# Optimization experiments

Hardware: AMD Instinct MI355X
Metric: run time of the kernel (lower is better)

Reference implementation:

```python
import jax, jax.numpy as jnp
import numpy as np


def setup_inputs() -> dict:
    key = jax.random.key(0)
    n_samples, n_points, dims = 16, 2048, 64
    h = jax.random.normal(key, (n_samples, n_points, dims), dtype=jnp.float32)
    return {"h": h, "K": 16}


def reference(h, K):
    """Pairwise squared distance + K nearest neighbors -> edge list.

    h : (n_samples, n_points, dims)
    Returns (knn_dist, dst, src):
      knn_dist : (n_samples, n_points, K) squared distances to the K nearest points
      dst, src : (n_samples*n_points*K,) int32 globally-offset edge endpoints
    """
    n_samples, n_points, _ = h.shape
    # d[b, i, j] = ||h[b,i]||^2 + ||h[b,j]||^2 - 2 <h[b,i], h[b,j]>
    x2s = jnp.sum(h * h, axis=-1, keepdims=True)          # (s, n, 1)
    d = x2s + jnp.swapaxes(x2s, -1, -2) - 2.0 * jnp.einsum('bnd,bmd->bnm', h, h)
    # smallest-K == top-K of negated distances (matches torch.topk largest=False order)
    neg_vals, k_indices = jax.lax.top_k(-d, K)            # (s, n, K)
    knn_dist = -neg_vals
    # edge list with per-sample node-id offsets (matches the torch flattening)
    src = jnp.broadcast_to(jnp.arange(n_points, dtype=k_indices.dtype)[None, :, None],
                           k_indices.shape)
    offset = (jnp.arange(n_samples, dtype=k_indices.dtype) * n_points)[:, None, None]
    dst = (k_indices + offset).reshape(-1)
    src = (src + offset).reshape(-1)
    return knn_dist, dst, src
```

## Files before the change

kernel.cpp:

```cpp
#include <hip/hip_runtime.h>
#include <hip/hip_fp16.h>
#include <cfloat>


typedef _Float16 half8 __attribute__((ext_vector_type(8)));
typedef float    f32x4 __attribute__((ext_vector_type(4)));

constexpr int NS = 16, NP = 2048, ND = 64, KK = 16;
constexpr int NWV = 4;
constexpr int NT  = NWV * 64;
constexpr int RB  = 32;
constexpr int ITN = RB / 16;
constexpr int JW  = NP / NWV;
constexpr int NJT = JW / 16;
constexpr int MS  = 17;
constexpr int SCB = 36;
constexpr int RCAP = 128;
constexpr int RSTR = RCAP + 1;
constexpr float MARGIN = 1.0f;

__global__ void prep_kernel(const float* __restrict__ h, float* __restrict__ x2,
                            _Float16* __restrict__ hh)
{
    int g = blockIdx.x * 128 + threadIdx.x;
    const float4* row = (const float4*)(h + (size_t)g * ND);
    int ph = g & 15;
    float a0 = 0.f, a1 = 0.f, a2 = 0.f, a3 = 0.f;
    #pragma unroll
    for (int k = 0; k < 16; ++k) {
        float4 v = row[(k + ph) & 15];
        a0 = fmaf(v.x, v.x, a0); a1 = fmaf(v.y, v.y, a1);
        a2 = fmaf(v.z, v.z, a2); a3 = fmaf(v.w, v.w, a3);
    }
    x2[g] = (a0 + a1) + (a2 + a3);
    _Float16* dst = hh + (size_t)g * ND;
    #pragma unroll
    for (int k = 0; k < 8; ++k) {
        float4 v0 = row[2 * k], v1 = row[2 * k + 1];
        half8 p;
        p[0] = (_Float16)v0.x; p[1] = (_Float16)v0.y;
        p[2] = (_Float16)v0.z; p[3] = (_Float16)v0.w;
        p[4] = (_Float16)v1.x; p[5] = (_Float16)v1.y;
        p[6] = (_Float16)v1.z; p[7] = (_Float16)v1.w;
        *(half8*)(dst + k * 8) = p;
    }
}

__device__ __forceinline__ bool lexlt(float a, int ja, float b, int jb)
{
    return (a < b) || (a == b && ja < jb);
}
__device__ __forceinline__ void insert16x(float (&d)[KK], int (&ix)[KK],
                                          float v, int j)
{
    #pragma unroll
    for (int p = KK - 1; p > 0; --p) {
        bool sh = lexlt(v, j, d[p - 1], ix[p - 1]);
        bool he = lexlt(v, j, d[p], ix[p]);
        float nd = sh ? d[p - 1] : (he ? v : d[p]);
        int   ni = sh ? ix[p - 1] : (he ? j : ix[p]);
        d[p] = nd; ix[p] = ni;
    }
    if (lexlt(v, j, d[0], ix[0])) { d[0] = v; ix[0] = j; }
}

__global__ __launch_bounds__(NT, 4)
void knn_mfma(const float* __restrict__ h, const _Float16* __restrict__ hh,
              const float* __restrict__ x2g, float* __restrict__ out)
{
    __shared__ __align__(16) float smem[8672];
    float* ldsx2  = smem;
    float* scb    = smem + 2048;
    float* mw     = smem + 4352;
    float* ldsthr = smem + 4480;
    int*   ring   = (int*)(smem + 4512);
    int*   rcnt   = (int*)(smem + 8640);
    float* md     = scb;
    int*   mi     = (int*)(scb + 1088);

    const int t   = threadIdx.x;
    const int ln  = t & 63;
    const int qd  = ln >> 4;
    const int cl  = ln & 15;
    const int q   = t >> 6;
    const int row = ln & 31;
    const int jh  = ln >> 5;
    const int s   = blockIdx.x >> 6;
    const int rb  = blockIdx.x & 63;
    const int rowbase = rb * RB;
    const float*    __restrict__ hs  = h  + (size_t)s * NP * ND;
    const _Float16* __restrict__ hhs = hh + (size_t)s * NP * ND;

    ((float4*)ldsx2)[t]       = ((const float4*)(x2g + s * NP))[t];
    ((float4*)ldsx2)[t + 256] = ((const float4*)(x2g + s * NP))[t + 256];
    if (t < RB) rcnt[t] = 0;

    half8 afr[ITN][2];
    #pragma unroll
    for (int it = 0; it < ITN; ++it) {
        const _Float16* ap = hhs + (size_t)(rowbase + it * 16 + cl) * ND + qd * 8;
        afr[it][0] = *(const half8*)(ap);
        afr[it][1] = *(const half8*)(ap + 32);
    }
    __syncthreads();

    const int jbase = q * JW;
    float* scbW = scb + q * (16 * SCB);

    float s1 = FLT_MAX, s2 = FLT_MAX, s3 = FLT_MAX, s4 = FLT_MAX;
    const int jro = jh * 8;
    for (int jt = 0; jt < NJT; ++jt) {
        const int j0 = jbase + jt * 16;
        const _Float16* bp = hhs + (size_t)(j0 + cl) * ND + qd * 8;
        half8 blo = *(const half8*)(bp);
        half8 bhi = *(const half8*)(bp + 32);
        float x2j = ldsx2[j0 + cl];

        f32x4 acc[ITN];
        #pragma unroll
        for (int it = 0; it < ITN; ++it) {
            acc[it] = __builtin_amdgcn_mfma_f32_16x16x32_f16(
                          afr[it][0], blo, (f32x4){0.f, 0.f, 0.f, 0.f}, 0, 0, 0);
            acc[it] = __builtin_amdgcn_mfma_f32_16x16x32_f16(
                          afr[it][1], bhi, acc[it], 0, 0, 0);
        }
        #pragma unroll
        for (int it = 0; it < ITN; ++it) {
            f32x4 w;
            #pragma unroll
            for (int r = 0; r < 4; ++r)
                w[r] = fmaf(-2.f, acc[it][r], x2j);
            *(f32x4*)(scbW + cl * SCB + it * 16 + qd * 4) = w;
        }
        #pragma unroll
        for (int u = 0; u < 8; ++u) {
            float v  = scbW[(jro + u) * SCB + row];
            float n1 = fminf(s1, v);
            float n2 = __builtin_amdgcn_fmed3f(s1, s2, v);
            float n3 = __builtin_amdgcn_fmed3f(s2, s3, v);
            float n4 = __builtin_amdgcn_fmed3f(s3, s4, v);
            s1 = n1; s2 = n2; s3 = n3; s4 = n4;
        }
    }
    {
        float o1 = __shfl(s1, row + 32);
        float o2 = __shfl(s2, row + 32);
        float o3 = __shfl(s3, row + 32);
        float o4 = __shfl(s4, row + 32);
        if (ln < 32) {
            float m1 = fminf(s1, o4), m2 = fminf(s2, o3);
            float m3 = fminf(s3, o2), m4 = fminf(s4, o1);
            mw[q * 32 + row] = fmaxf(fmaxf(m1, m2), fmaxf(m3, m4));
        }
    }
    __syncthreads();
    if (q == 0 && ln < 32) {
        float m0 = mw[row], m1 = mw[32 + row];
        float m2 = mw[64 + row], m3 = mw[96 + row];
        ldsthr[row] = fmaxf(fmaxf(m0, m1), fmaxf(m2, m3)) + MARGIN;
    }
    __syncthreads();

    float thrv[ITN * 4];
    #pragma unroll
    for (int it = 0; it < ITN; ++it)
        #pragma unroll
        for (int r = 0; r < 4; ++r)
            thrv[it * 4 + r] = ldsthr[it * 16 + qd * 4 + r];

    for (int jt = 0; jt < NJT; ++jt) {
        const int j0 = jbase + jt * 16;
        const _Float16* bp = hhs + (size_t)(j0 + cl) * ND + qd * 8;
        half8 blo = *(const half8*)(bp);
        half8 bhi = *(const half8*)(bp + 32);
        float x2j = ldsx2[j0 + cl];

        f32x4 acc[ITN];
        #pragma unroll
        for (int it = 0; it < ITN; ++it) {
            acc[it] = __builtin_amdgcn_mfma_f32_16x16x32_f16(
                          afr[it][0], blo, (f32x4){0.f, 0.f, 0.f, 0.f}, 0, 0, 0);
            acc[it] = __builtin_amdgcn_mfma_f32_16x16x32_f16(
                          afr[it][1], bhi, acc[it], 0, 0, 0);
        }
        #pragma unroll
        for (int it = 0; it < ITN; ++it) {
            #pragma unroll
            for (int r = 0; r < 4; ++r) {
                float d2 = fmaf(-2.f, acc[it][r], x2j);
                if (d2 < thrv[it * 4 + r]) {
                    int rw = it * 16 + qd * 4 + r;
                    int slot = atomicAdd(&rcnt[rw], 1);
                    if (slot < RCAP) ring[rw * RSTR + slot] = j0 + cl;
                }
            }
        }
    }
    __syncthreads();

    const int myrow = rowbase + row;
    float4 A[16];
    {
        const float4* ra = (const float4*)(hs + (size_t)myrow * ND);
        #pragma unroll
        for (int k = 0; k < 16; ++k) A[k] = ra[k];
    }
    float x2i;
    {
        float a0 = 0.f, a1 = 0.f, a2 = 0.f, a3 = 0.f;
        #pragma unroll
        for (int k = 0; k < 16; ++k) {
            a0 = fmaf(A[k].x, A[k].x, a0); a1 = fmaf(A[k].y, A[k].y, a1);
            a2 = fmaf(A[k].z, A[k].z, a2); a3 = fmaf(A[k].w, A[k].w, a3);
        }
        x2i = (a0 + a1) + (a2 + a3);
    }
    float dist[KK]; int idx[KK];
    #pragma unroll
    for (int k = 0; k < KK; ++k) { dist[k] = FLT_MAX; idx[k] = 0; }

    const int cntR = min(rcnt[row], RCAP);
    const int w8 = q * 2 + jh;
    #pragma unroll 1
    for (int k = w8; k < cntR; k += 8) {
        int j = ring[row * RSTR + k];
        const float4* cv = (const float4*)(hs + (size_t)j * ND);
        float a0 = 0.f, a1 = 0.f, a2 = 0.f, a3 = 0.f;
        #pragma unroll
        for (int kk = 0; kk < 16; ++kk) {
            float4 c = cv[kk];
            a0 = fmaf(A[kk].x, c.x, a0); a1 = fmaf(A[kk].y, c.y, a1);
            a2 = fmaf(A[kk].z, c.z, a2); a3 = fmaf(A[kk].w, c.w, a3);
        }
        float dotv = (a0 + a1) + (a2 + a3);
        float d2 = fmaf(-2.0f, dotv, x2i + ldsx2[j]);
        if (lexlt(d2, j, dist[KK - 1], idx[KK - 1]))
            insert16x(dist, idx, d2, j);
    }

    #pragma unroll 1
    for (int k = 0; k < KK; ++k) {
        float v  = __shfl(dist[k], row + 32);
        int   jv = __shfl(idx[k],  row + 32);
        bool need = (ln < 32) && lexlt(v, jv, dist[KK - 1], idx[KK - 1]);
        if (!__any(need)) break;
        if (need) insert16x(dist, idx, v, jv);
    }
    __syncthreads();
    #pragma unroll 1
    for (int lvl = 0; lvl < 2; ++lvl) {
        const int step = 1 << lvl;
        const int m    = (step << 1) - 1;
        const bool pub = ((q & m) == step) && ln < 32;
        const int reg  = q >> (lvl + 1);
        if (pub) {
            #pragma unroll
            for (int k = 0; k < KK; ++k) {
                md[(reg * RB + row) * MS + k] = dist[k];
                mi[(reg * RB + row) * MS + k] = idx[k];
            }
        }
        __syncthreads();
        if ((q & m) == 0) {
            #pragma unroll 1
            for (int k = 0; k < KK; ++k) {
                float v  = md[(reg * RB + row) * MS + k];
                int   jv = mi[(reg * RB + row) * MS + k];
                bool need = (ln < 32) && lexlt(v, jv, dist[KK - 1], idx[KK - 1]);
                if (!__any(need)) break;
                if (need) insert16x(dist, idx, v, jv);
            }
        }
        __syncthreads();
    }

    if (q == 0 && ln < 32) {
        const int off = s * NP;
        const size_t rg = (size_t)off + myrow;
        float* o0 = out + rg * KK;
        float* o1 = out + (size_t)NS * NP * KK + rg * KK;
        float* o2 = out + (size_t)2 * NS * NP * KK + rg * KK;
        #pragma unroll
        for (int k = 0; k < KK; ++k) o0[k] = dist[k];
        #pragma unroll
        for (int k = 0; k < KK; ++k) o1[k] = (float)(idx[k] + off);
        #pragma unroll
        for (int k = 0; k < KK; ++k) o2[k] = (float)(off + myrow);
    }
}

extern "C" void kernel_launch(void* const* d_in, const int* in_sizes, int n_in,
                              void* d_out, int out_size, void* d_ws, size_t ws_size,
                              hipStream_t stream)
{
    const float* h = (const float*)d_in[0];
    float* out = (float*)d_out;
    float*    x2 = (float*)d_ws;
    _Float16* hh = (_Float16*)(x2 + NS * NP);

    hipLaunchKernelGGL(prep_kernel, dim3(NS * NP / 128), dim3(128), 0, stream,
                       h, x2, hh);
    hipLaunchKernelGGL(knn_mfma, dim3(NS * (NP / RB)), dim3(NT), 0, stream,
                       h, hh, x2, out);
}
```

Baseline: 216.7 us.

## Transpose MFMA operands to keep per-row top-4 in registers, drop LDS staging

Swaps the MFMA A/B operands so each lane's accumulator holds four candidate columns for a fixed query row. The running top-4 threshold can then be kept in registers per row tile instead of staging distances through a shared-memory scratch buffer and re-reading them. Partial top-4 lists are merged across lane groups with xor shuffles, and the filter pass compares against one threshold per row. The two main loops are unrolled by two and the prep kernel uses 256-thread blocks. The cost is more registers for the per-row-tile threshold state.

```diff
diff --git a/kernel.cpp b/kernel.cpp
--- a/kernel.cpp
+++ b/kernel.cpp
@@ -14,7 +14,6 @@
 constexpr int JW  = NP / NWV;
 constexpr int NJT = JW / 16;
 constexpr int MS  = 17;
-constexpr int SCB = 36;
 constexpr int RCAP = 128;
 constexpr int RSTR = RCAP + 1;
 constexpr float MARGIN = 1.0f;
@@ -22,7 +21,7 @@
 __global__ void prep_kernel(const float* __restrict__ h, float* __restrict__ x2,
                             _Float16* __restrict__ hh)
 {
-    int g = blockIdx.x * 128 + threadIdx.x;
+    int g = blockIdx.x * 256 + threadIdx.x;
     const float4* row = (const float4*)(h + (size_t)g * ND);
     int ph = g & 15;
     float a0 = 0.f, a1 = 0.f, a2 = 0.f, a3 = 0.f;
@@ -68,15 +67,14 @@
 void knn_mfma(const float* __restrict__ h, const _Float16* __restrict__ hh,
               const float* __restrict__ x2g, float* __restrict__ out)
 {
-    __shared__ __align__(16) float smem[8672];
+    __shared__ __align__(16) float smem[8544];
     float* ldsx2  = smem;
-    float* scb    = smem + 2048;
-    float* mw     = smem + 4352;
-    float* ldsthr = smem + 4480;
-    int*   ring   = (int*)(smem + 4512);
-    int*   rcnt   = (int*)(smem + 8640);
-    float* md     = scb;
-    int*   mi     = (int*)(scb + 1088);
+    float* mw     = smem + 2048;
+    float* ldsthr = smem + 2176;
+    int*   rcnt   = (int*)(smem + 2208);
+    int*   ring   = (int*)(smem + 2240);
+    float* md     = smem + 6368;
+    int*   mi     = (int*)(smem + 7456);
 
     const int t   = threadIdx.x;
     const int ln  = t & 63;
@@ -95,63 +93,67 @@
     ((float4*)ldsx2)[t + 256] = ((const float4*)(x2g + s * NP))[t + 256];
     if (t < RB) rcnt[t] = 0;
 
-    half8 afr[ITN][2];
+    half8 ifr[ITN][2];
     #pragma unroll
     for (int it = 0; it < ITN; ++it) {
         const _Float16* ap = hhs + (size_t)(rowbase + it * 16 + cl) * ND + qd * 8;
-        afr[it][0] = *(const half8*)(ap);
-        afr[it][1] = *(const half8*)(ap + 32);
+        ifr[it][0] = *(const half8*)(ap);
+        ifr[it][1] = *(const half8*)(ap + 32);
     }
     __syncthreads();
 
     const int jbase = q * JW;
-    float* scbW = scb + q * (16 * SCB);
-
-    float s1 = FLT_MAX, s2 = FLT_MAX, s3 = FLT_MAX, s4 = FLT_MAX;
-    const int jro = jh * 8;
+
+    float t1[ITN], t2[ITN], t3[ITN], t4[ITN];
+    #pragma unroll
+    for (int it = 0; it < ITN; ++it)
+        { t1[it] = FLT_MAX; t2[it] = FLT_MAX; t3[it] = FLT_MAX; t4[it] = FLT_MAX; }
+
+    #pragma unroll 2
     for (int jt = 0; jt < NJT; ++jt) {
         const int j0 = jbase + jt * 16;
         const _Float16* bp = hhs + (size_t)(j0 + cl) * ND + qd * 8;
-        half8 blo = *(const half8*)(bp);
-        half8 bhi = *(const half8*)(bp + 32);
-        float x2j = ldsx2[j0 + cl];
-
-        f32x4 acc[ITN];
+        half8 jlo = *(const half8*)(bp);
+        half8 jhi = *(const half8*)(bp + 32);
+        f32x4 x2q = *(const f32x4*)(ldsx2 + j0 + qd * 4);
+
         #pragma unroll
         for (int it = 0; it < ITN; ++it) {
-            acc[it] = __builtin_amdgcn_mfma_f32_16x16x32_f16(
-                          afr[it][0], blo, (f32x4){0.f, 0.f, 0.f, 0.f}, 0, 0, 0);
-            acc[it] = __builtin_amdgcn_mfma_f32_16x16x32_f16(
-                          afr[it][1], bhi, acc[it], 0, 0, 0);
-        }
-        #pragma unroll
-        for (int it = 0; it < ITN; ++it) {
-            f32x4 w;
+            f32x4 acc;
+            acc = __builtin_amdgcn_mfma_f32_16x16x32_f16(
+                      jlo, ifr[it][0], (f32x4){0.f, 0.f, 0.f, 0.f}, 0, 0, 0);
+            acc = __builtin_amdgcn_mfma_f32_16x16x32_f16(
+                      jhi, ifr[it][1], acc, 0, 0, 0);
             #pragma unroll
-            for (int r = 0; r < 4; ++r)
-                w[r] = fmaf(-2.f, acc[it][r], x2j);
-            *(f32x4*)(scbW + cl * SCB + it * 16 + qd * 4) = w;
-        }
-        #pragma unroll
-        for (int u = 0; u < 8; ++u) {
-            float v  = scbW[(jro + u) * SCB + row];
-            float n1 = fminf(s1, v);
-            float n2 = __builtin_amdgcn_fmed3f(s1, s2, v);
-            float n3 = __builtin_amdgcn_fmed3f(s2, s3, v);
-            float n4 = __builtin_amdgcn_fmed3f(s3, s4, v);
-            s1 = n1; s2 = n2; s3 = n3; s4 = n4;
-        }
-    }
-    {
-        float o1 = __shfl(s1, row + 32);
-        float o2 = __shfl(s2, row + 32);
-        float o3 = __shfl(s3, row + 32);
-        float o4 = __shfl(s4, row + 32);
-        if (ln < 32) {
-            float m1 = fminf(s1, o4), m2 = fminf(s2, o3);
-            float m3 = fminf(s3, o2), m4 = fminf(s4, o1);
-            mw[q * 32 + row] = fmaxf(fmaxf(m1, m2), fmaxf(m3, m4));
-        }
+            for (int r = 0; r < 4; ++r) {
+                float v  = fmaf(-2.f, acc[r], x2q[r]);
+                float n1 = fminf(t1[it], v);
+                float n2 = __builtin_amdgcn_fmed3f(t1[it], t2[it], v);
+                float n3 = __builtin_amdgcn_fmed3f(t2[it], t3[it], v);
+                float n4 = __builtin_amdgcn_fmed3f(t3[it], t4[it], v);
+                t1[it] = n1; t2[it] = n2; t3[it] = n3; t4[it] = n4;
+            }
+        }
+    }
+
+    #pragma unroll
+    for (int it = 0; it < ITN; ++it) {
+        #pragma unroll
+        for (int lvl = 0; lvl < 2; ++lvl) {
+            const int mask = 16 << lvl;
+            float b1 = __shfl_xor(t1[it], mask), b2 = __shfl_xor(t2[it], mask);
+            float b3 = __shfl_xor(t3[it], mask), b4 = __shfl_xor(t4[it], mask);
+            float m1 = fminf(t1[it], b4), m2 = fminf(t2[it], b3);
+            float m3 = fminf(t3[it], b2), m4 = fminf(t4[it], b1);
+            float u1 = fminf(m1, m3), u3 = fmaxf(m1, m3);
+            float u2 = fminf(m2, m4), u4 = fmaxf(m2, m4);
+            t1[it] = fminf(u1, u2); t2[it] = fmaxf(u1, u2);
+            t3[it] = fminf(u3, u4); t4[it] = fmaxf(u3, u4);
+        }
+    }
+    if (qd == 0) {
+        mw[q * 32 + cl]      = t4[0];
+        mw[q * 32 + 16 + cl] = t4[1];
     }
     __syncthreads();
     if (q == 0 && ln < 32) {
@@ -161,37 +163,32 @@
     }
     __syncthreads();
 
-    float thrv[ITN * 4];
-    #pragma unroll
-    for (int it = 0; it < ITN; ++it)
-        #pragma unroll
-        for (int r = 0; r < 4; ++r)
-            thrv[it * 4 + r] = ldsthr[it * 16 + qd * 4 + r];
-
+    float thrv[ITN];
+    #pragma unroll
+    for (int it = 0; it < ITN; ++it) thrv[it] = ldsthr[it * 16 + cl];
+
+    #pragma unroll 2
     for (int jt = 0; jt < NJT; ++jt) {
         const int j0 = jbase + jt * 16;
         const _Float16* bp = hhs + (size_t)(j0 + cl) * ND + qd * 8;
-        half8 blo = *(const half8*)(bp);
-        half8 bhi = *(const half8*)(bp + 32);
-        float x2j = ldsx2[j0 + cl];
-
-        f32x4 acc[ITN];
+        half8 jlo = *(const half8*)(bp);
+        half8 jhi = *(const half8*)(bp + 32);
+        f32x4 x2q = *(const f32x4*)(ldsx2 + j0 + qd * 4);
+
         #pragma unroll
         for (int it = 0; it < ITN; ++it) {
-            acc[it] = __builtin_amdgcn_mfma_f32_16x16x32_f16(
-                          afr[it][0], blo, (f32x4){0.f, 0.f, 0.f, 0.f}, 0, 0, 0);
-            acc[it] = __builtin_amdgcn_mfma_f32_16x16x32_f16(
-                          afr[it][1], bhi, acc[it], 0, 0, 0);
-        }
-        #pragma unroll
-        for (int it = 0; it < ITN; ++it) {
+            f32x4 acc;
+            acc = __builtin_amdgcn_mfma_f32_16x16x32_f16(
+                      jlo, ifr[it][0], (f32x4){0.f, 0.f, 0.f, 0.f}, 0, 0, 0);
+            acc = __builtin_amdgcn_mfma_f32_16x16x32_f16(
+                      jhi, ifr[it][1], acc, 0, 0, 0);
             #pragma unroll
             for (int r = 0; r < 4; ++r) {
-                float d2 = fmaf(-2.f, acc[it][r], x2j);
-                if (d2 < thrv[it * 4 + r]) {
-                    int rw = it * 16 + qd * 4 + r;
+                float d2 = fmaf(-2.f, acc[r], x2q[r]);
+                if (d2 < thrv[it]) {
+                    int rw = it * 16 + cl;
                     int slot = atomicAdd(&rcnt[rw], 1);
-                    if (slot < RCAP) ring[rw * RSTR + slot] = j0 + cl;
+                    if (slot < RCAP) ring[rw * RSTR + slot] = j0 + qd * 4 + r;
                 }
             }
         }
@@ -298,7 +295,7 @@
     float*    x2 = (float*)d_ws;
     _Float16* hh = (_Float16*)(x2 + NS * NP);
 
-    hipLaunchKernelGGL(prep_kernel, dim3(NS * NP / 128), dim3(128), 0, stream,
+    hipLaunchKernelGGL(prep_kernel, dim3(NS * NP / 256), dim3(256), 0, stream,
                        h, x2, hh);
     hipLaunchKernelGGL(knn_mfma, dim3(NS * (NP / RB)), dim3(NT), 0, stream,
                        h, hh, x2, out);
```

Result: no change. 219.7 us (+1.4%).
